# Optimization experiments

Hardware: AMD Instinct MI355X
Metric: run time of the kernel (lower is better)

The kernel has to match this reference:

```python
import jax, jax.numpy as jnp
import numpy as np

B, L, F, H, HDE, E, V, MH, MW, TOUT = 64, 2, 512, 512, 512, 512, 94, 6, 40, 30
V2 = V + 2          # vocab + START/END + NULL slots
T = TOUT + 2        # decode steps
HW = MH * MW
START = V + 1
END = V + 1


def setup_inputs() -> dict:
    key = jax.random.key(0)
    ks = jax.random.split(key, 20)
    s = 0.05  # weight scale for numerical stability
    n = lambda k, shape: jax.random.normal(k, shape, jnp.float32) * s
    d = {}
    d['conv_f'] = jax.random.normal(ks[0], (B, F, MH, MW), jnp.float32)
    d['target'] = jax.random.randint(ks[1], (B, TOUT), 0, 95, dtype=jnp.int32)
    d['w_ih_en'] = n(ks[2], (L, 4 * H, F))
    d['w_hh_en'] = n(ks[3], (L, 4 * H, H))
    d['b_ih_en'] = n(ks[4], (L, 4 * H))
    d['b_hh_en'] = n(ks[5], (L, 4 * H))
    d['embed_w'] = n(ks[6], (V2, H))
    d['w_ih_de'] = n(ks[7], (L, 4 * HDE, H))
    d['w_hh_de'] = n(ks[8], (L, 4 * HDE, HDE))
    d['b_ih_de'] = n(ks[9], (L, 4 * HDE))
    d['b_hh_de'] = n(ks[10], (L, 4 * HDE))
    d['att_wh'] = n(ks[11], (E, HDE))
    d['att_bh'] = n(ks[12], (E,))
    d['att_conv_w'] = n(ks[13], (E, F, 3, 3))
    d['att_conv_b'] = n(ks[14], (E,))
    d['att_wv'] = n(ks[15], (1, E))
    d['att_bv'] = n(ks[16], (1,))
    d['out_w'] = n(ks[17], (V2, HDE + F))
    d['out_b'] = n(ks[18], (V2,))
    return d


def _lstm_cell(x, h, c, wih, whh, bih, bhh):
    # PyTorch gate order: i, f, g, o
    g = x @ wih.T + h @ whh.T + bih + bhh
    i, f, gg, o = jnp.split(g, 4, axis=-1)
    c_new = jax.nn.sigmoid(f) * c + jax.nn.sigmoid(i) * jnp.tanh(gg)
    h_new = jax.nn.sigmoid(o) * jnp.tanh(c_new)
    return h_new, c_new


def _forward(conv_f, target, w_ih_en, w_hh_en, b_ih_en, b_hh_en, embed_w,
             w_ih_de, w_hh_de, b_ih_de, b_hh_de, att_wh, att_bh,
             att_conv_w, att_conv_b, att_wv, att_bv, out_w, out_b):
    # ---- encoder: maxpool over full height, then 2-layer LSTM over width ----
    x_seq = jnp.max(conv_f, axis=2).transpose(2, 0, 1)  # [W, B, F]

    def enc_step(carry, xt):
        h, c = carry
        inp = xt
        hs, cs = [], []
        for l in range(L):
            hl, cl = _lstm_cell(inp, h[l], c[l], w_ih_en[l], w_hh_en[l],
                                b_ih_en[l], b_hh_en[l])
            inp = hl
            hs.append(hl); cs.append(cl)
        return (jnp.stack(hs), jnp.stack(cs)), inp

    z = jnp.zeros((L, B, H), conv_f.dtype)
    _, enc_out = jax.lax.scan(enc_step, (z, z), x_seq)
    holistic = enc_out[-1]  # [B, H]

    # ---- attention: conv_f embedding computed ONCE (invariant across steps) ----
    xe = jax.lax.conv_general_dilated(
        conv_f, att_conv_w, (1, 1), 'SAME',
        dimension_numbers=('NCHW', 'OIHW', 'NCHW')) + att_conv_b[None, :, None, None]
    x_em = xe.reshape(B, E, HW).transpose(0, 2, 1)       # [B, HW, E]
    cf_flat = conv_f.reshape(B, F, HW).transpose(0, 2, 1)  # [B, HW, F]

    # ---- decoder inputs: t=0 holistic, t>=1 embed(gt_with_start[:, t-1]) ----
    gt = jnp.concatenate(
        [jnp.full((B, 1), START, dtype=target.dtype), target], axis=1)  # [B, T-1]
    xs = jnp.concatenate([holistic[None], embed_w[gt.T]], axis=0)  # [T, B, H]

    def dec_step(carry, xt):
        h, c = carry
        inp = xt
        hs, cs = [], []
        for l in range(L):
            hl, cl = _lstm_cell(inp, h[l], c[l], w_ih_de[l], w_hh_de[l],
                                b_ih_de[l], b_hh_de[l])
            inp = hl
            hs.append(hl); cs.append(cl)
        hlast = inp  # [B, HDE]
        g_em = hlast @ att_wh.T + att_bh                    # [B, E]
        feat = jnp.tanh(x_em + g_em[:, None, :])            # [B, HW, E] (dropout=identity)
        e = feat @ att_wv[0] + att_bv[0]                    # [B, HW]
        alpha = jax.nn.softmax(e, axis=-1)
        att = jnp.einsum('bw,bwf->bf', alpha, cf_flat)      # [B, F]
        logits = jnp.concatenate([hlast, att], axis=-1) @ out_w.T + out_b
        scores = jax.nn.log_softmax(logits, axis=-1)        # [B, V2]
        return (jnp.stack(hs), jnp.stack(cs)), scores

    zd = jnp.zeros((B, HDE), conv_f.dtype)
    z0 = jnp.stack([zd] * L)
    _, out_tbv = jax.lax.scan(dec_step, (z0, z0), xs)  # [T, B, V2]
    out = out_tbv.transpose(1, 0, 2)                    # [B, T, V2]

    # ---- build l_target: [0, target..., 0] with first padding 0 -> END ----
    l_target = jnp.zeros((B, T), jnp.int32).at[:, 1:-1].set(target)
    j = jnp.argmax(l_target[:, 1:] == 0, axis=1) + 1  # first zero at col>=1 (always exists)
    l_target = l_target.at[jnp.arange(B), j].set(END)

    # ---- masked NLL loss ----
    lt = l_target.reshape(-1)
    nll = -out.reshape(-1, V2)[jnp.arange(B * T), lt]
    mask = (lt != 0).astype(out.dtype)
    return jnp.sum(nll * mask) / jnp.sum(mask)


def reference(conv_f, target, w_ih_en, w_hh_en, b_ih_en, b_hh_en, embed_w,
              w_ih_de, w_hh_de, b_ih_de, b_hh_de, att_wh, att_bh,
              att_conv_w, att_conv_b, att_wv, att_bv, out_w, out_b):
    return _forward(conv_f, target, w_ih_en, w_hh_en, b_ih_en, b_hh_en, embed_w,
                    w_ih_de, w_hh_de, b_ih_de, b_hh_de, att_wh, att_bh,
                    att_conv_w, att_conv_b, att_wv, att_bv, out_w, out_b)
```

## Files before the change

### kernel.cpp

```cpp
#include <hip/hip_runtime.h>

typedef __fp16 f16;
typedef __fp16 f16x4 __attribute__((ext_vector_type(4)));
typedef __fp16 f16x8 __attribute__((ext_vector_type(8)));
typedef float  f32x4 __attribute__((ext_vector_type(4)));
typedef unsigned long long ull;

#define DEV static __device__ __forceinline__

DEV f32x4 mfma16(f16x4 a, f16x4 b, f32x4 c) {
  return __builtin_amdgcn_mfma_f32_16x16x16f16(a, b, c, 0, 0, 0);
}
DEV f16x4 lo4(f16x8 v) { return __builtin_shufflevector(v, v, 0, 1, 2, 3); }
DEV f16x4 hi4(f16x8 v) { return __builtin_shufflevector(v, v, 4, 5, 6, 7); }
DEV float sigf(float x) { return 1.f / (1.f + __expf(-x)); }
DEV float tanh_(float x) { float e = __expf(2.f * x); return 1.f - 2.f / (e + 1.f); }

union U8 { float4 f4; float2 f2[2]; };
union H2 { unsigned u; f16 h[2]; };
union H4 { ull u; f16 h[4]; f16x4 v; };

#define HB 32768

DEV ull ldU(const ull* p) {
  return __hip_atomic_load(p, __ATOMIC_RELAXED, __HIP_MEMORY_SCOPE_AGENT);
}
DEV unsigned ldF(const unsigned* p) {
  return __hip_atomic_load(p, __ATOMIC_RELAXED, __HIP_MEMORY_SCOPE_AGENT);
}
DEV void stU32(unsigned* p, unsigned v) {
  __hip_atomic_store(p, v, __ATOMIC_RELAXED, __HIP_MEMORY_SCOPE_AGENT);
}
DEV void stU64(ull* p, ull v) {
  __hip_atomic_store(p, v, __ATOMIC_RELAXED, __HIP_MEMORY_SCOPE_AGENT);
}

DEV void wait8(const unsigned* line, unsigned tgt) {
  if (threadIdx.x < 8)
    while (ldF(line + threadIdx.x * 16) < tgt) {}
  __syncthreads();
}

DEV void signalDone(unsigned* line, int slot) {
  asm volatile("s_waitcnt vmcnt(0)" ::: "memory");
  __syncthreads();
  if (threadIdx.x == 0)
    __hip_atomic_fetch_add(line + slot * 16, 1u, __ATOMIC_RELAXED, __HIP_MEMORY_SCOPE_AGENT);
}

DEV void stageRow(const f16* __restrict__ s, f16* __restrict__ dstRow, int ch) {
  U8 u0, u1;
  u0.f4 = *(const float4*)s;
  u1.f4 = *(const float4*)(s + 8);
  *(float2*)(dstRow +  0 + ch * 4) = u0.f2[0];
  *(float2*)(dstRow + 16 + ch * 4) = u0.f2[1];
  *(float2*)(dstRow + 32 + ch * 4) = u1.f2[0];
  *(float2*)(dstRow + 48 + ch * 4) = u1.f2[1];
}

DEV void stageAp(const f16* __restrict__ rowSrc, f16 (*A)[64][72], int tid) {
  int ch = tid & 3;
  const f16* s = rowSrc + ch * 16;
#pragma unroll
  for (int c = 0; c < 8; ++c)
    stageRow(s + c * 64, &A[c][tid >> 2][0], ch);
}

DEV void stageAu(const ull* __restrict__ srcU, f16 (*A)[64][72], int tid) {
  int row = tid >> 2, ch = tid & 3;
  const ull* s = srcU + row * 128 + ch * 4;
#pragma unroll
  for (int c = 0; c < 8; ++c) {
    ull d0 = ldU(s + c * 16 + 0);
    ull d1 = ldU(s + c * 16 + 1);
    ull d2 = ldU(s + c * 16 + 2);
    ull d3 = ldU(s + c * 16 + 3);
    f16* d = &A[c][row][0];
    *(ull*)(d +  0 + ch * 4) = d0;
    *(ull*)(d + 16 + ch * 4) = d1;
    *(ull*)(d + 32 + ch * 4) = d2;
    *(ull*)(d + 48 + ch * 4) = d3;
  }
}

DEV void kloop32(const f16 (*Wt)[32][72], const f16 (*A)[64][72],
                 int mh, int ns, int m16, int g4, f32x4 acc[2]) {
#pragma unroll
  for (int c = 0; c < 8; ++c) {
#pragma unroll
    for (int half = 0; half < 2; ++half) {
      f16x8 bf = *(const f16x8*)&Wt[c][ns * 16 + m16][g4 * 16 + half * 8];
      f16x4 bl = lo4(bf), bh = hi4(bf);
#pragma unroll
      for (int mt = 0; mt < 2; ++mt) {
        f16x8 af = *(const f16x8*)&A[c][mh * 32 + mt * 16 + m16][g4 * 16 + half * 8];
        acc[mt] = mfma16(lo4(af), bl, acc[mt]);
        acc[mt] = mfma16(hi4(af), bh, acc[mt]);
      }
    }
  }
}

DEV void kloop64(const f16* Wg, const f16 (*A)[64][72],
                 int nsG, int m16, int g4, f32x4 acc[4]) {
#pragma unroll
  for (int c = 0; c < 8; ++c) {
#pragma unroll
    for (int half = 0; half < 2; ++half) {
      f16x8 bf = *(const f16x8*)&Wg[((size_t)(c * 64 + nsG * 16 + m16)) * 72 + g4 * 16 + half * 8];
      f16x4 bl = lo4(bf), bh = hi4(bf);
#pragma unroll
      for (int mt = 0; mt < 4; ++mt) {
        f16x8 af = *(const f16x8*)&A[c][mt * 16 + m16][g4 * 16 + half * 8];
        acc[mt] = mfma16(lo4(af), bl, acc[mt]);
        acc[mt] = mfma16(hi4(af), bh, acc[mt]);
      }
    }
  }
}

DEV void convTile(char* smem, int tile, const f16* __restrict__ cfT,
                  const f16* __restrict__ wc9, const float* __restrict__ cb,
                  f16* __restrict__ xemH) {
  f16 (*At)[40] = (f16(*)[40])smem;
  f16 (*Bt)[40] = (f16(*)[40])(smem + 19200);
  const int t = threadIdx.x, lane = t & 63, w = t >> 6;
  const int b = tile >> 2, eb = (tile & 3) * 128;
  const int m16 = lane & 15, g4 = lane >> 4;
  f32x4 acc[15][2] = {};

  for (int kr = 0; kr < 9; ++kr) {
    int dh = kr / 3 - 1, dw = kr % 3 - 1;
    for (int f0 = 0; f0 < 512; f0 += 32) {
      __syncthreads();
      if (t < 240) {
        int hh = t / 40 + dh, ww = t % 40 + dw;
        if (hh >= 0 && hh < 6 && ww >= 0 && ww < 40) {
          const f16* s = cfT + ((size_t)(b * 240 + hh * 40 + ww) * 512 + f0);
          U8 u0, u1, u2, u3;
          u0.f4 = *(const float4*)s;        u1.f4 = *(const float4*)(s + 8);
          u2.f4 = *(const float4*)(s + 16); u3.f4 = *(const float4*)(s + 24);
          *(float2*)&At[t][ 0] = u0.f2[0];
          *(float2*)&At[t][ 8] = u0.f2[1];
          *(float2*)&At[t][16] = u1.f2[0];
          *(float2*)&At[t][24] = u1.f2[1];
          *(float2*)&At[t][ 4] = u2.f2[0];
          *(float2*)&At[t][12] = u2.f2[1];
          *(float2*)&At[t][20] = u3.f2[0];
          *(float2*)&At[t][28] = u3.f2[1];
        } else {
          float2 z = make_float2(0.f, 0.f);
          *(float2*)&At[t][ 0] = z; *(float2*)&At[t][ 8] = z;
          *(float2*)&At[t][16] = z; *(float2*)&At[t][24] = z;
          *(float2*)&At[t][ 4] = z; *(float2*)&At[t][12] = z;
          *(float2*)&At[t][20] = z; *(float2*)&At[t][28] = z;
        }
      }
      {
        int n = t >> 1, ch = t & 1;
        const f16* s = wc9 + (size_t)(eb + n) * 4608 + kr * 512 + f0 + ch * 16;
        U8 u0, u1;
        u0.f4 = *(const float4*)s; u1.f4 = *(const float4*)(s + 8);
        *(float2*)&Bt[n][ 0 + ch * 4] = u0.f2[0];
        *(float2*)&Bt[n][ 8 + ch * 4] = u0.f2[1];
        *(float2*)&Bt[n][16 + ch * 4] = u1.f2[0];
        *(float2*)&Bt[n][24 + ch * 4] = u1.f2[1];
      }
      __syncthreads();
      f16x8 b0 = *(const f16x8*)&Bt[w * 32 + m16][g4 * 8];
      f16x8 b1v = *(const f16x8*)&Bt[w * 32 + 16 + m16][g4 * 8];
      f16x4 b0l = lo4(b0), b0h = hi4(b0), b1l = lo4(b1v), b1h = hi4(b1v);
#pragma unroll
      for (int mt = 0; mt < 15; ++mt) {
        f16x8 af = *(const f16x8*)&At[mt * 16 + m16][g4 * 8];
        f16x4 al = lo4(af), ah = hi4(af);
        acc[mt][0] = mfma16(al, b0l, acc[mt][0]);
        acc[mt][1] = mfma16(al, b1l, acc[mt][1]);
        acc[mt][0] = mfma16(ah, b0h, acc[mt][0]);
        acc[mt][1] = mfma16(ah, b1h, acc[mt][1]);
      }
    }
  }
#pragma unroll
  for (int nt = 0; nt < 2; ++nt) {
    int e = eb + w * 32 + nt * 16 + m16;
    float bias = cb[e];
#pragma unroll
    for (int mt = 0; mt < 15; ++mt)
#pragma unroll
      for (int r = 0; r < 4; ++r) {
        int p = mt * 16 + g4 * 4 + r;
        xemH[((size_t)(b * 240 + p)) * 512 + e] = (f16)(acc[mt][nt][r] + bias);
      }
  }
}

__global__ __launch_bounds__(256) void k_prep(
    const float* __restrict__ att_cw, f16* __restrict__ wc9,
    const float* __restrict__ s0, const float* __restrict__ s1,
    const float* __restrict__ s2, const float* __restrict__ s3,
    f16* __restrict__ d0, f16* __restrict__ d1,
    f16* __restrict__ d2, f16* __restrict__ d3,
    const float* __restrict__ awhS, const float* __restrict__ embS,
    const float* __restrict__ outwS,
    f16* __restrict__ awhD, f16* __restrict__ embD, f16* __restrict__ outwD,
    unsigned* __restrict__ z0, unsigned* __restrict__ z1, unsigned* __restrict__ z2,
    unsigned* __restrict__ z3, unsigned* __restrict__ z4, unsigned* __restrict__ z5)
{
  const int bid = blockIdx.x, tid = threadIdx.x;
  if (bid < 512) {
    __shared__ float s[4608];
    const int e = bid;
    for (int i = tid; i < 4608; i += 256) s[i] = att_cw[(size_t)e * 4608 + i];
    __syncthreads();
    for (int j = tid; j < 4608; j += 256) {
      int rr = j >> 9, f = j & 511;
      wc9[(size_t)e * 4608 + j] = (f16)s[f * 9 + rr];
    }
  } else if (bid < 8704) {
    int i = (bid - 512) * 256 + tid;
    int sel = i >> 19, j = i & 524287;
    const float* s = sel == 0 ? s0 : sel == 1 ? s1 : sel == 2 ? s2 : s3;
    f16* d = sel == 0 ? d0 : sel == 1 ? d1 : sel == 2 ? d2 : d3;
    float4 v = ((const float4*)s)[j];
    f16x4 o = { (f16)v.x, (f16)v.y, (f16)v.z, (f16)v.w };
    *(f16x4*)(d + (size_t)j * 4) = o;
  } else if (bid < 9104) {
    int i = (bid - 8704) * 256 + tid;
    const float* s; f16* d; int j;
    if (i < 65536) { s = awhS; d = awhD; j = i; }
    else if (i < 65536 + 12288) { s = embS; d = embD; j = i - 65536; }
    else if (i < 65536 + 12288 + 24576) { s = outwS; d = outwD; j = i - 65536 - 12288; }
    else return;
    float4 v = ((const float4*)s)[j];
    f16x4 o = { (f16)v.x, (f16)v.y, (f16)v.z, (f16)v.w };
    *(f16x4*)(d + (size_t)j * 4) = o;
  } else {
    int i = (bid - 9104) * 256 + tid;
    int sel = i >> 14, j = i & 16383;
    unsigned* p = sel == 0 ? z0 : sel == 1 ? z1 : sel == 2 ? z2 :
                  sel == 3 ? z3 : sel == 4 ? z4 : z5;
    p[j] = 0;
  }
}

__global__ __launch_bounds__(256) void k_cfmx(
// ... 36 lines not shown
__global__ __launch_bounds__(256) void k_gemmX(
    const f16* __restrict__ A, const f16* __restrict__ W,
    const float* __restrict__ b1, const float* __restrict__ b2,
    f16* __restrict__ C)
{
  __shared__ f16 At[64][72];
  __shared__ f16 Bt[64][72];
  const int t = threadIdx.x, lane = t & 63, g = t >> 6;
  f32x4 acc[4] = {};
  const int m16 = lane & 15, g4 = lane >> 4;
  const size_t arow0 = (size_t)blockIdx.x * 64;

  for (int k0 = 0; k0 < 512; k0 += 64) {
    __syncthreads();
    { int row = t >> 2, ch = t & 3;
      stageRow(A + (arow0 + row) * 512 + k0 + ch * 16, &At[row][0], ch); }
    { int row = t >> 2, ch = t & 3;
      stageRow(W + ((size_t)blockIdx.y * 64 + row) * 512 + k0 + ch * 16, &Bt[row][0], ch); }
    __syncthreads();
#pragma unroll
    for (int half = 0; half < 2; ++half) {
      f16x8 bf = *(const f16x8*)&Bt[g * 16 + m16][g4 * 16 + half * 8];
      f16x4 bl = lo4(bf), bh = hi4(bf);
#pragma unroll
      for (int mt = 0; mt < 4; ++mt) {
        f16x8 af = *(const f16x8*)&At[mt * 16 + m16][g4 * 16 + half * 8];
        acc[mt] = mfma16(lo4(af), bl, acc[mt]);
        acc[mt] = mfma16(hi4(af), bh, acc[mt]);
      }
    }
  }
  int e = blockIdx.y * 64 + g * 16 + m16;
  float bias = b1[e] + b2[e];
#pragma unroll
  for (int mt = 0; mt < 4; ++mt)
#pragma unroll
    for (int r = 0; r < 4; ++r)
      C[(arow0 + mt * 16 + g4 * 4 + r) * 2048 + e] = (f16)(acc[mt][r] + bias);
}

__global__ __launch_bounds__(256, 1) void k_lstm(
    int T, int mode,
    const f16* __restrict__ G0, const f16* __restrict__ whh0,
    const f16* __restrict__ wih1, const f16* __restrict__ whh1,
    const float* __restrict__ bih1, const float* __restrict__ bhh1,
    f16* __restrict__ h0seq, f16* __restrict__ h1seq,
    unsigned* __restrict__ cnt,
    const f16* __restrict__ cfT, const f16* __restrict__ wc9,
    const float* __restrict__ cb, f16* __restrict__ xemH, int convBase,
    f16* __restrict__ X0de, const f16* __restrict__ wihD0,
    const float* __restrict__ bihD0, const float* __restrict__ bhhD0,
    const f16* __restrict__ emb, const int* __restrict__ tgt,
    const f16* __restrict__ x_t0,
    const f16* __restrict__ awh, const float* __restrict__ gbias, f16* __restrict__ gAll)
{
  __shared__ __align__(16) char smem[147456];
  const int tid = threadIdx.x, lane = tid & 63, w = tid >> 6;
  const int m16 = lane & 15, g4 = lane >> 4;
  const int bid = blockIdx.x;

  if (bid < 32) {
    f16 (*sW)[64][72] = (f16(*)[64][72])smem;
    f16 (*sA)[64][72] = (f16(*)[64][72])(smem + 73728);
    float* sG = (float*)(smem + 73728);
    const int utile = bid;
    { int r = tid >> 2, ch = tid & 3;
      int grow = (r >> 4) * 512 + utile * 16 + (r & 15);
      for (int c = 0; c < 8; ++c)
        stageRow(whh0 + (size_t)grow * 512 + c * 64 + ch * 16, &sW[c][r][0], ch);
    }
    const int pb = tid >> 2, uq = tid & 3;
    float cst[4] = {0.f, 0.f, 0.f, 0.f};
    for (int t = 0; t < T; ++t) {
      if (t > 0) wait8(cnt + (size_t)(t - 1) * 128, 4);
      else if (mode == 1) wait8(cnt + (size_t)(2 * T) * 128, 1);
      const f16* gpp = G0 + (size_t)(t * 64 + pb) * 2048 + utile * 16 + uq * 4;
      H4 gI, gF, gG, gO;
      gI.v = *(const f16x4*)(gpp);
      gF.v = *(const f16x4*)(gpp + 512);
      gG.v = *(const f16x4*)(gpp + 1024);
      gO.v = *(const f16x4*)(gpp + 1536);
      stageAu((const ull*)h0seq + (size_t)t * 8192, sA, tid);
      __syncthreads();
      f32x4 acc[4] = {};
      kloop64((const f16*)sW, sA, w, m16, g4, acc);
      __syncthreads();
#pragma unroll
      for (int mt = 0; mt < 4; ++mt)
#pragma unroll
        for (int r = 0; r < 4; ++r)
          sG[((size_t)w * 64 + mt * 16 + g4 * 4 + r) * 17 + m16] = acc[mt][r];
      __syncthreads();
      {
        H4 outp;
#pragma unroll
        for (int j = 0; j < 4; ++j) {
          int u = uq * 4 + j;
          float gi = sG[(0 * 64 + pb) * 17 + u] + (float)gI.h[j];
          float gf = sG[(1 * 64 + pb) * 17 + u] + (float)gF.h[j];
          float gg = sG[(2 * 64 + pb) * 17 + u] + (float)gG.h[j];
          float go = sG[(3 * 64 + pb) * 17 + u] + (float)gO.h[j];
          float cn = sigf(gf) * cst[j] + sigf(gi) * tanh_(gg);
          float hn = sigf(go) * tanh_(cn);
          cst[j] = cn;
          outp.h[j] = (f16)hn;
        }
        stU64((ull*)h0seq + (size_t)(t + 1) * 8192 + pb * 128 + utile * 4 + uq, outp.u);
// ... 31 lines not shown
      else       __syncthreads();
      ull rg[8][4];
      { const ull* s1p = (const ull*)h1seq + (size_t)t * 8192 + (tid >> 2) * 128 + (tid & 3) * 4;
#pragma unroll
        for (int c = 0; c < 8; ++c)
#pragma unroll
          for (int q = 0; q < 4; ++q) rg[c][q] = ldU(s1p + c * 16 + q);
      }
      f32x4 acc[2] = {};
      kloop32(sW2[0], sA, mh, ns, m16, g4, acc);
      __syncthreads();
      { int row = tid >> 2, ch = tid & 3;
#pragma unroll
        for (int c = 0; c < 8; ++c) {
          f16* d = &sA[c][row][0];
          *(ull*)(d +  0 + ch * 4) = rg[c][0];
          *(ull*)(d + 16 + ch * 4) = rg[c][1];
          *(ull*)(d + 32 + ch * 4) = rg[c][2];
          *(ull*)(d + 48 + ch * 4) = rg[c][3];
        }
      }
      __syncthreads();
      kloop32(sW2[1], sA, mh, ns, m16, g4, acc);
      __syncthreads();
      { int nl = ns * 16 + m16;
#pragma unroll
        for (int mt = 0; mt < 2; ++mt)
#pragma unroll
          for (int r = 0; r < 4; ++r) {
            int b = mh * 32 + mt * 16 + g4 * 4 + r;
            sG[((nl >> 3) * 64 + b) * 9 + (nl & 7)] = acc[mt][r];
          }
      }
      __syncthreads();
      {
        H2 outp;
#pragma unroll
        for (int j = 0; j < 2; ++j) {
          int u = pup * 2 + j;
          float gi = sG[(0 * 64 + pb) * 9 + u] + badd[0][j];
          float gf = sG[(1 * 64 + pb) * 9 + u] + badd[1][j];
          float gg = sG[(2 * 64 + pb) * 9 + u] + badd[2][j];
          float go = sG[(3 * 64 + pb) * 9 + u] + badd[3][j];
          float cn = sigf(gf) * cst[j] + sigf(gi) * tanh_(gg);
          float hn = sigf(go) * tanh_(cn);
          cst[j] = cn;
          outp.h[j] = (f16)hn;
        }
        stU32((unsigned*)h1seq + (size_t)(t + 1) * 16384 + pb * 256 + utile * 4 + pup, outp.u);
      }
      signalDone(line1 + (size_t)t * 128, bid & 7);
    }
  } else if (bid < 224) {
    convTile(smem, convBase + bid - 96, cfT, wc9, cb, xemH);
  } else if (mode == 0) {
    const int rid = bid - 224;
    f16 (*sW)[64][72] = (f16(*)[64][72])smem;
    f16 (*sA)[64][72] = (f16(*)[64][72])(smem + 73728);
    { int r = tid >> 2, ch = tid & 3;
      for (int c = 0; c < 8; ++c)
        stageRow(wihD0 + (size_t)(rid * 64 + r) * 512 + c * 64 + ch * 16, &sW[c][r][0], ch);
    }
    const int e = rid * 64 + w * 16 + m16;
    const float bias_e = bihD0[e] + bhhD0[e];
    const int arow = tid >> 2;
    __syncthreads();
    for (int tt = 1; tt < 32; ++tt) {
      const f16* rowSrc = (tt == 1) ? emb + (size_t)95 * 512
                                    : emb + (size_t)tgt[arow * 30 + tt - 2] * 512;
      stageAp(rowSrc, sA, tid);
      __syncthreads();
      f32x4 acc[4] = {};
      kloop64((const f16*)sW, sA, w, m16, g4, acc);
      __syncthreads();
#pragma unroll
      for (int mt = 0; mt < 4; ++mt)
#pragma unroll
        for (int r = 0; r < 4; ++r)
          X0de[((size_t)tt * 64 + mt * 16 + g4 * 4 + r) * 2048 + e] = (f16)(acc[mt][r] + bias_e);
      __syncthreads();
    }
  } else {
    const int g = bid - 224;
    f16* sWg = (f16*)smem;
    f16 (*sA)[64][72] = (f16(*)[64][72])(smem + 73728);
    stageAp(x_t0 + (size_t)(tid >> 2) * 512, sA, tid);
    __syncthreads();
    for (int q = 0; q < 4; ++q) {
      const int rid = g * 4 + q;
      { int r = tid >> 2, ch = tid & 3;
        for (int c = 0; c < 8; ++c)
          stageRow(wihD0 + (size_t)(rid * 64 + r) * 512 + c * 64 + ch * 16,
                   sWg + ((size_t)(c * 64 + r)) * 72, ch);
      }
      __syncthreads();
      f32x4 acc[4] = {};
      kloop64(sWg, sA, w, m16, g4, acc);
      const int e = rid * 64 + w * 16 + m16;
      const float bias_e = bihD0[e] + bhhD0[e];
#pragma unroll
      for (int mt = 0; mt < 4; ++mt)
#pragma unroll
        for (int r = 0; r < 4; ++r)
          X0de[((size_t)(mt * 16 + g4 * 4 + r)) * 2048 + e] = (f16)(acc[mt][r] + bias_e);
      __syncthreads();
    }
    signalDone(cnt + (size_t)(2 * T) * 128, g);
    { int r = tid >> 2, ch = tid & 3;
      for (int c = 0; c < 8; ++c)
        stageRow(awh + (size_t)(g * 64 + r) * 512 + c * 64 + ch * 16,
                 sWg + ((size_t)(c * 64 + r)) * 72, ch);
    }
    const int e = g * 64 + w * 16 + m16;
    const float gb = gbias[e];
    __syncthreads();
    unsigned* line1 = cnt + (size_t)T * 128;
    for (int t = 0; t < T; ++t) {
      wait8(line1 + (size_t)t * 128, 8);
      stageAu((const ull*)h1seq + (size_t)(t + 1) * 8192, sA, tid);
      __syncthreads();
      f32x4 acc[4] = {};
      kloop64(sWg, sA, w, m16, g4, acc);
      __syncthreads();
#pragma unroll
      for (int mt = 0; mt < 4; ++mt)
#pragma unroll
        for (int r = 0; r < 4; ++r)
          gAll[(size_t)(t * 64 + mt * 16 + g4 * 4 + r) * 512 + e] = (f16)(acc[mt][r] + gb);
    }
  }
}


__global__ __launch_bounds__(256) void k_scoreAll(
    const f16* __restrict__ xemH, const f16* __restrict__ gAll,
    const float* __restrict__ wv, float* __restrict__ esc)
{
  __shared__ f16 sX[20][512];
  const int tid = threadIdx.x, lane = tid & 63, w = tid >> 6;
  const int tile = blockIdx.x, b = blockIdx.y;
  for (int i = tid; i < 20 * 64; i += 256) {
    int row = i >> 6, seg = i & 63;
    *(f16x8*)&sX[row][seg * 8] =
        *(const f16x8*)(xemH + ((size_t)(b * 240 + tile * 20 + row)) * 512 + seg * 8);
  }
  float w8[8];
  { const float4* wp = (const float4*)(wv + lane * 8);
    float4 wa = wp[0], wb = wp[1];
    w8[0] = wa.x; w8[1] = wa.y; w8[2] = wa.z; w8[3] = wa.w;
    w8[4] = wb.x; w8[5] = wb.y; w8[6] = wb.z; w8[7] = wb.w; }
  __syncthreads();
  for (int t = 0; t < 32; ++t) {
    f16x8 gv = *(const f16x8*)(gAll + ((size_t)(t * 64 + b)) * 512 + lane * 8);
    float g8[8];
#pragma unroll
    for (int j = 0; j < 8; ++j) g8[j] = (float)gv[j];
#pragma unroll
    for (int i = 0; i < 5; ++i) {
      int rr = i * 4 + w;
      f16x8 xv = *(const f16x8*)&sX[rr][lane * 8];
      float s = 0.f;
#pragma unroll
      for (int j = 0; j < 8; ++j) s += tanh_((float)xv[j] + g8[j]) * w8[j];
#pragma unroll
      for (int m = 32; m; m >>= 1) s += __shfl_xor(s, m);
      if (lane == 0) esc[((size_t)(t * 64 + b)) * 240 + tile * 20 + rr] = s;
    }
  }
}

__global__ __launch_bounds__(256) void k_smctx(
    const float* __restrict__ esc, const f16* __restrict__ cfT,
    const f16* __restrict__ h1seq, f16* __restrict__ ctx)
{
  __shared__ float aAl[8][240];
  const int tid = threadIdx.x, lane = tid & 63, w = tid >> 6;
  const int tq = blockIdx.x, b = blockIdx.y;
  for (int half = 0; half < 2; ++half) {
    int tt = w + half * 4;
    int t = tq * 8 + tt;
    const float* er = esc + ((size_t)(t * 64 + b)) * 240;
    float v[4];
    float mx = -1e30f;
#pragma unroll
    for (int q = 0; q < 4; ++q) {
      int p = lane + q * 64;
      v[q] = (p < 240) ? er[p] : -1e30f;
      mx = fmaxf(mx, v[q]);
    }
#pragma unroll
    for (int m = 32; m; m >>= 1) mx = fmaxf(mx, __shfl_xor(mx, m));
    float sum = 0.f;
#pragma unroll
    for (int q = 0; q < 4; ++q) { v[q] = __expf(v[q] - mx); sum += v[q]; }
#pragma unroll
    for (int m = 32; m; m >>= 1) sum += __shfl_xor(sum, m);
    float inv = 1.f / sum;
#pragma unroll
    for (int q = 0; q < 4; ++q) {
      int p = lane + q * 64;
      if (p < 240) aAl[tt][p] = v[q] * inv;
    }
  }
  __syncthreads();
  float acc[8][2] = {};
  const f16* cb = cfT + (size_t)b * 240 * 512;
  for (int p = 0; p < 240; ++p) {
    H2 cw; cw.u = *(const unsigned*)(cb + (size_t)p * 512 + tid * 2);
    float c0 = (float)cw.h[0], c1 = (float)cw.h[1];
#pragma unroll
    for (int tt = 0; tt < 8; ++tt) {
      float a = aAl[tt][p];
      acc[tt][0] += a * c0;
      acc[tt][1] += a * c1;
    }
  }
#pragma unroll
  for (int tt = 0; tt < 8; ++tt) {
    int t = tq * 8 + tt;
    size_t r = (size_t)(t * 64 + b);
    H2 o; o.h[0] = (f16)acc[tt][0]; o.h[1] = (f16)acc[tt][1];
    *(unsigned*)(ctx + r * 1024 + 512 + tid * 2) = o.u;
    *(unsigned*)(ctx + r * 1024 + tid * 2) =
        *(const unsigned*)(h1seq + (size_t)(t + 1) * HB + b * 512 + tid * 2);
  }
}

__global__ __launch_bounds__(256) void k_logit(
    const f16* __restrict__ A,
    const f16* __restrict__ W,
    const float* __restrict__ bias, const int* __restrict__ tgt,
    float* __restrict__ nllb)
{
  __shared__ f16 At[64][72];
  __shared__ f16 Bt[2][64][72];
  __shared__ float sL[64][100];
  const int tid = threadIdx.x, lane = tid & 63, g = tid >> 6;
  const int m16 = lane & 15, g4 = lane >> 4;
  const int t = blockIdx.x;
  const size_t arow0 = (size_t)t * 64;
  f32x4 acc[2][4] = {};

  for (int k0 = 0; k0 < 1024; k0 += 64) {
    __syncthreads();
    { int row = tid >> 2, ch = tid & 3;
      stageRow(A + (arow0 + row) * 1024 + k0 + ch * 16, &At[row][0], ch);
      stageRow(W + (size_t)row * 1024 + k0 + ch * 16, &Bt[0][row][0], ch);
      stageRow(W + (size_t)(64 + row) * 1024 + k0 + ch * 16, &Bt[1][row][0], ch); }
    __syncthreads();
#pragma unroll
    for (int n2 = 0; n2 < 2; ++n2)
#pragma unroll
      for (int half = 0; half < 2; ++half) {
        f16x8 bf = *(const f16x8*)&Bt[n2][g * 16 + m16][g4 * 16 + half * 8];
        f16x4 bl = lo4(bf), bh = hi4(bf);
#pragma unroll
        for (int mt = 0; mt < 4; ++mt) {
          f16x8 af = *(const f16x8*)&At[mt * 16 + m16][g4 * 16 + half * 8];
          acc[n2][mt] = mfma16(lo4(af), bl, acc[n2][mt]);
          acc[n2][mt] = mfma16(hi4(af), bh, acc[n2][mt]);
        }
      }
  }
  __syncthreads();
#pragma unroll
  for (int n2 = 0; n2 < 2; ++n2) {
    int e = n2 * 64 + g * 16 + m16;
    if (e < 96) {
      float be = bias[e];
#pragma unroll
      for (int mt = 0; mt < 4; ++mt)
#pragma unroll
        for (int r = 0; r < 4; ++r)
          sL[mt * 16 + g4 * 4 + r][e] = acc[n2][mt][r] + be;
    }
  }
  __syncthreads();
  if (tid < 64) {
    int b = tid;
    int jj = 31;
    for (int q = 1; q <= 30; ++q)
      if (tgt[b * 30 + q - 1] == 0) { jj = q; break; }
    int tok = (t == 0 || t == 31) ? 0 : tgt[b * 30 + t - 1];
    if (t == jj) tok = 95;
    float val = 0.f;
    if (tok != 0) {
      float mx = -1e30f;
      for (int j = 0; j < 96; ++j) mx = fmaxf(mx, sL[b][j]);
      float s = 0.f;
      for (int j = 0; j < 96; ++j) s += __expf(sL[b][j] - mx);
      val = mx + __logf(s) - sL[b][tok];
    }
    nllb[t * 64 + b] = val;
  }
}

__global__ void k_loss(const float* __restrict__ nllb, const int* __restrict__ tgt,
                       float* __restrict__ out) {
  __shared__ float sa[256], sb[256];
  int tid = threadIdx.x;
  float a = 0.f, m = 0.f;
  for (int i = tid; i < 2048; i += 256) a += nllb[i];
  if (tid < 64) {
    int b = tid;
    int jj = 31;
    for (int q = 1; q <= 30; ++q)
      if (tgt[b * 30 + q - 1] == 0) { jj = q; break; }
    int cnt = 0;
    for (int t = 1; t <= 30; ++t) {
      int v = tgt[b * 30 + t - 1];
      if (t == jj) v = 95;
      if (v != 0) ++cnt;
    }
    if (jj == 31) ++cnt;
    m = (float)cnt;
  }
  sa[tid] = a; sb[tid] = m; __syncthreads();
  for (int s = 128; s; s >>= 1) { if (tid < s) { sa[tid] += sa[tid + s]; sb[tid] += sb[tid + s]; } __syncthreads(); }
  if (tid == 0) out[0] = sa[0] / sb[0];
}


extern "C" void kernel_launch(void* const* d_in, const int* in_sizes, int n_in,
                              void* d_out, int out_size, void* d_ws, size_t ws_size,
                              hipStream_t stream) {
  (void)in_sizes; (void)n_in; (void)out_size; (void)ws_size;
  const float* conv_f = (const float*)d_in[0];
  const int*   target = (const int*)d_in[1];
  const float* wih_en = (const float*)d_in[2];
  const float* whh_en = (const float*)d_in[3];
  const float* bih_en = (const float*)d_in[4];
  const float* bhh_en = (const float*)d_in[5];
  const float* embed  = (const float*)d_in[6];
  const float* wih_de = (const float*)d_in[7];
  const float* whh_de = (const float*)d_in[8];
  const float* bih_de = (const float*)d_in[9];
  const float* bhh_de = (const float*)d_in[10];
  const float* att_wh = (const float*)d_in[11];
  const float* att_bh = (const float*)d_in[12];
  const float* att_cw = (const float*)d_in[13];
  const float* att_cb = (const float*)d_in[14];
  const float* att_wv = (const float*)d_in[15];
  const float* out_w  = (const float*)d_in[17];
  const float* out_b  = (const float*)d_in[18];
  float* out = (float*)d_out;

  size_t o = 0;
  char* base = (char*)d_ws;
  auto take = [&](size_t bytes) -> void* {
    void* p = base + o;
    o += (bytes + 255) & ~(size_t)255;
    return p;
  };
  const size_t WSZ = (size_t)2048 * 512;
  f16* wihEn = (f16*)take(2 * WSZ * 2);
  f16* whhEn = (f16*)take(2 * WSZ * 2);
  f16* wihDe = (f16*)take(2 * WSZ * 2);
  f16* whhDe = (f16*)take(2 * WSZ * 2);
  f16* awh   = (f16*)take((size_t)512 * 512 * 2);
  f16* emb   = (f16*)take((size_t)96 * 512 * 2);
  f16* wc9   = (f16*)take((size_t)512 * 4608 * 2);
  f16* cfT   = (f16*)take((size_t)64 * 240 * 512 * 2);
  f16* xseq  = (f16*)take((size_t)40 * 64 * 512 * 2);
  f16* xemH  = (f16*)take((size_t)64 * 240 * 512 * 2);
  f16* outwH = (f16*)take((size_t)128 * 1024 * 2);
  f16* X0en  = (f16*)take((size_t)2560 * 2048 * 2);
  f16* X0de  = (f16*)take((size_t)2048 * 2048 * 2);
  f16* h0seqE = (f16*)take((size_t)41 * HB * 2);
  f16* h1seqE = (f16*)take((size_t)41 * HB * 2);
  f16* h0seqD = (f16*)take((size_t)33 * HB * 2);
  f16* h1seqD = (f16*)take((size_t)33 * HB * 2);
  f16* gAll   = (f16*)take((size_t)2048 * 512 * 2);
  float* nllb = (float*)take((size_t)2048 * 4);
  unsigned* cntE = (unsigned*)take(65536);
  unsigned* cntD = (unsigned*)take(65536);
  float* escAll = (float*)X0en;
  f16*   ctxAll = X0de;

  k_cfmx<<<dim3(8, 64), 256, 0, stream>>>(conv_f, cfT, xseq);
  k_prep<<<9488, 256, 0, stream>>>(att_cw, wc9,
                                   wih_en, whh_en, wih_de, whh_de,
                                   wihEn, whhEn, wihDe, whhDe,
                                   att_wh, embed, out_w, awh, emb, outwH,
                                   (unsigned*)h0seqE, (unsigned*)h1seqE,
                                   (unsigned*)h0seqD, (unsigned*)h1seqD, cntE, cntD);

  k_gemmX<<<dim3(40, 32), 256, 0, stream>>>(xseq, wihEn, bih_en, bhh_en, X0en);
  k_lstm<<<256, 256, 0, stream>>>(40, 0, X0en, whhEn, wihEn + WSZ, whhEn + WSZ,
                                  bih_en + 2048, bhh_en + 2048, h0seqE, h1seqE, cntE,
                                  cfT, wc9, att_cb, xemH, 0,
                                  X0de, wihDe, bih_de, bhh_de, emb, target,
                                  nullptr, nullptr, nullptr, nullptr);

  k_lstm<<<232, 256, 0, stream>>>(32, 1, X0de, whhDe, wihDe + WSZ, whhDe + WSZ,
                                  bih_de + 2048, bhh_de + 2048, h0seqD, h1seqD, cntD,
                                  cfT, wc9, att_cb, xemH, 128,
                                  X0de, wihDe, bih_de, bhh_de, emb, target,
                                  h1seqE + (size_t)40 * HB,
                                  awh, att_bh, gAll);

  k_scoreAll<<<dim3(12, 64), 256, 0, stream>>>(xemH, gAll, att_wv, escAll);
  k_smctx<<<dim3(4, 64), 256, 0, stream>>>(escAll, cfT, h1seqD, ctxAll);
  k_logit<<<32, 256, 0, stream>>>(ctxAll, outwH, out_b, target, nllb);
  k_loss<<<1, 256, 0, stream>>>(nllb, target, out);
}
```

Before: 769.8 us.

## Fuse attention score, softmax-context, logits and loss into persistent decoder kernel

The four trailing kernels (score, softmax/context, logit, loss) are moved into the tail of the mode-1 persistent LSTM kernel. Blocks pick up tasks in a grid-stride loop and wait on atomic counters that conv tiles, the gAll producer and each stage signal, so the attention tail can start as soon as its inputs exist. Cross-block data goes through agent-scope atomic loads and stores. The aim is to remove four launch gaps and overlap the tail with conv work. The cost is spin-waits and relaxed-atomic memory traffic, and ctxAll is moved to a new buffer so it no longer aliases X0de.

```diff
diff --git a/kernel.cpp b/kernel.cpp
--- a/kernel.cpp
+++ b/kernel.cpp
@@ -19,6 +19,7 @@
 union U8 { float4 f4; float2 f2[2]; };
 union H2 { unsigned u; f16 h[2]; };
 union H4 { ull u; f16 h[4]; f16x4 v; };
+union U32F { unsigned u; float f; };
 
 #define HB 32768
 
@@ -46,6 +47,13 @@
   __syncthreads();
   if (threadIdx.x == 0)
     __hip_atomic_fetch_add(line + slot * 16, 1u, __ATOMIC_RELAXED, __HIP_MEMORY_SCOPE_AGENT);
+}
+
+DEV void signalOne(unsigned* ctr) {
+  asm volatile("s_waitcnt vmcnt(0)" ::: "memory");
+  __syncthreads();
+  if (threadIdx.x == 0)
+    __hip_atomic_fetch_add(ctr, 1u, __ATOMIC_RELAXED, __HIP_MEMORY_SCOPE_AGENT);
 }
 
 DEV void stageRow(const f16* __restrict__ s, f16* __restrict__ dstRow, int ch) {
@@ -119,15 +127,13 @@
   }
 }
 
-DEV void convTile(char* smem, int tile, const f16* __restrict__ cfT,
-                  const f16* __restrict__ wc9, const float* __restrict__ cb,
-                  f16* __restrict__ xemH) {
+DEV void convCore(char* smem, int tile, const f16* __restrict__ cfT,
+                  const f16* __restrict__ wc9, f32x4 acc[15][2]) {
   f16 (*At)[40] = (f16(*)[40])smem;
   f16 (*Bt)[40] = (f16(*)[40])(smem + 19200);
   const int t = threadIdx.x, lane = t & 63, w = t >> 6;
   const int b = tile >> 2, eb = (tile & 3) * 128;
   const int m16 = lane & 15, g4 = lane >> 4;
-  f32x4 acc[15][2] = {};
 
   for (int kr = 0; kr < 9; ++kr) {
     int dh = kr / 3 - 1, dw = kr % 3 - 1;
@@ -181,6 +187,16 @@
       }
     }
   }
+}
+
+DEV void convTileC(char* smem, int tile, const f16* __restrict__ cfT,
+                   const f16* __restrict__ wc9, const float* __restrict__ cb,
+                   f16* __restrict__ xemH) {
+  f32x4 acc[15][2] = {};
+  convCore(smem, tile, cfT, wc9, acc);
+  const int t = threadIdx.x, lane = t & 63, w = t >> 6;
+  const int b = tile >> 2, eb = (tile & 3) * 128;
+  const int m16 = lane & 15, g4 = lane >> 4;
 #pragma unroll
   for (int nt = 0; nt < 2; ++nt) {
     int e = eb + w * 32 + nt * 16 + m16;
@@ -192,6 +208,36 @@
         int p = mt * 16 + g4 * 4 + r;
         xemH[((size_t)(b * 240 + p)) * 512 + e] = (f16)(acc[mt][nt][r] + bias);
       }
+  }
+}
+
+DEV void convTileA(char* smem, int tile, const f16* __restrict__ cfT,
+                   const f16* __restrict__ wc9, const float* __restrict__ cb,
+                   f16* __restrict__ xemH) {
+  f32x4 acc[15][2] = {};
+  convCore(smem, tile, cfT, wc9, acc);
+  const int t = threadIdx.x, lane = t & 63, w = t >> 6;
+  const int b = tile >> 2, eb = (tile & 3) * 128;
+  const int m16 = lane & 15, g4 = lane >> 4;
+  f16 (*sC)[132] = (f16(*)[132])smem;
+  __syncthreads();
+#pragma unroll
+  for (int nt = 0; nt < 2; ++nt) {
+    int e = eb + w * 32 + nt * 16 + m16;
+    float bias = cb[e];
+#pragma unroll
+    for (int mt = 0; mt < 15; ++mt)
+#pragma unroll
+      for (int r = 0; r < 4; ++r)
+        sC[mt * 16 + g4 * 4 + r][w * 32 + nt * 16 + m16] = (f16)(acc[mt][nt][r] + bias);
+  }
+  __syncthreads();
+#pragma unroll
+  for (int k = 0; k < 30; ++k) {
+    int id = t + k * 256;
+    int row = id >> 5, chk = id & 31;
+    H4 pk; pk.v = *(const f16x4*)&sC[row][chk * 4];
+    stU64((ull*)xemH + (size_t)(b * 240 + row) * 128 + (eb >> 2) + chk, pk.u);
   }
 }
 
@@ -334,7 +380,11 @@
     const float* __restrict__ bihD0, const float* __restrict__ bhhD0,
     const f16* __restrict__ emb, const int* __restrict__ tgt,
     const f16* __restrict__ x_t0,
-    const f16* __restrict__ awh, const float* __restrict__ gbias, f16* __restrict__ gAll)
+    const f16* __restrict__ awh, const float* __restrict__ gbias, f16* __restrict__ gAll,
+    const float* __restrict__ wv, const f16* __restrict__ outwH,
+    const float* __restrict__ outb,
+    float* __restrict__ escAll, f16* __restrict__ ctxAll,
+    float* __restrict__ nllb, float* __restrict__ out)
 {
   __shared__ __align__(16) char smem[147456];
   const int tid = threadIdx.x, lane = tid & 63, w = tid >> 6;
@@ -472,7 +522,13 @@
       signalDone(line1 + (size_t)t * 128, bid & 7);
     }
   } else if (bid < 224) {
-    convTile(smem, convBase + bid - 96, cfT, wc9, cb, xemH);
+    if (mode == 0) {
+      convTileC(smem, convBase + bid - 96, cfT, wc9, cb, xemH);
+    } else {
+      int tile = convBase + bid - 96;
+      convTileA(smem, tile, cfT, wc9, cb, xemH);
+      signalOne(cnt + 8320 + (tile >> 2) * 16);
+    }
   } else if (mode == 0) {
     const int rid = bid - 224;
     f16 (*sW)[64][72] = (f16(*)[64][72])smem;
@@ -504,6 +560,7 @@
     const int g = bid - 224;
     f16* sWg = (f16*)smem;
     f16 (*sA)[64][72] = (f16(*)[64][72])(smem + 73728);
+    f16 (*sC)[72] = (f16(*)[72])(smem + 73728 + 36864);
     stageAp(x_t0 + (size_t)(tid >> 2) * 512, sA, tid);
     __syncthreads();
     for (int q = 0; q < 4; ++q) {
@@ -546,198 +603,238 @@
       for (int mt = 0; mt < 4; ++mt)
 #pragma unroll
         for (int r = 0; r < 4; ++r)
-          gAll[(size_t)(t * 64 + mt * 16 + g4 * 4 + r) * 512 + e] = (f16)(acc[mt][r] + gb);
-    }
-  }
-}
-
-
-__global__ __launch_bounds__(256) void k_scoreAll(
-    const f16* __restrict__ xemH, const f16* __restrict__ gAll,
-    const float* __restrict__ wv, float* __restrict__ esc)
-{
-  __shared__ f16 sX[20][512];
-  const int tid = threadIdx.x, lane = tid & 63, w = tid >> 6;
-  const int tile = blockIdx.x, b = blockIdx.y;
-  for (int i = tid; i < 20 * 64; i += 256) {
-    int row = i >> 6, seg = i & 63;
-    *(f16x8*)&sX[row][seg * 8] =
-        *(const f16x8*)(xemH + ((size_t)(b * 240 + tile * 20 + row)) * 512 + seg * 8);
-  }
-  float w8[8];
-  { const float4* wp = (const float4*)(wv + lane * 8);
-    float4 wa = wp[0], wb = wp[1];
-    w8[0] = wa.x; w8[1] = wa.y; w8[2] = wa.z; w8[3] = wa.w;
-    w8[4] = wb.x; w8[5] = wb.y; w8[6] = wb.z; w8[7] = wb.w; }
+          sC[mt * 16 + g4 * 4 + r][w * 16 + m16] = (f16)(acc[mt][r] + gb);
+      __syncthreads();
+#pragma unroll
+      for (int k = 0; k < 4; ++k) {
+        int id = tid + k * 256;
+        int row = id >> 4, chk = id & 15;
+        H4 pk; pk.v = *(const f16x4*)&sC[row][chk * 4];
+        stU64((ull*)gAll + (size_t)(t * 64 + row) * 128 + g * 16 + chk, pk.u);
+      }
+      __syncthreads();
+    }
+    signalOne(cnt + 9344);
+  }
+
+  if (mode == 0) return;
+
   __syncthreads();
-  for (int t = 0; t < 32; ++t) {
-    f16x8 gv = *(const f16x8*)(gAll + ((size_t)(t * 64 + b)) * 512 + lane * 8);
-    float g8[8];
-#pragma unroll
-    for (int j = 0; j < 8; ++j) g8[j] = (float)gv[j];
-#pragma unroll
-    for (int i = 0; i < 5; ++i) {
-      int rr = i * 4 + w;
-      f16x8 xv = *(const f16x8*)&sX[rr][lane * 8];
-      float s = 0.f;
-#pragma unroll
-      for (int j = 0; j < 8; ++j) s += tanh_((float)xv[j] + g8[j]) * w8[j];
-#pragma unroll
-      for (int m = 32; m; m >>= 1) s += __shfl_xor(s, m);
-      if (lane == 0) esc[((size_t)(t * 64 + b)) * 240 + tile * 20 + rr] = s;
-    }
-  }
-}
-
-__global__ __launch_bounds__(256) void k_smctx(
-    const float* __restrict__ esc, const f16* __restrict__ cfT,
-    const f16* __restrict__ h1seq, f16* __restrict__ ctx)
-{
-  __shared__ float aAl[8][240];
-  const int tid = threadIdx.x, lane = tid & 63, w = tid >> 6;
-  const int tq = blockIdx.x, b = blockIdx.y;
-  for (int half = 0; half < 2; ++half) {
-    int tt = w + half * 4;
-    int t = tq * 8 + tt;
-    const float* er = esc + ((size_t)(t * 64 + b)) * 240;
-    float v[4];
-    float mx = -1e30f;
-#pragma unroll
-    for (int q = 0; q < 4; ++q) {
-      int p = lane + q * 64;
-      v[q] = (p < 240) ? er[p] : -1e30f;
-      mx = fmaxf(mx, v[q]);
-    }
-#pragma unroll
-    for (int m = 32; m; m >>= 1) mx = fmaxf(mx, __shfl_xor(mx, m));
-    float sum = 0.f;
-#pragma unroll
-    for (int q = 0; q < 4; ++q) { v[q] = __expf(v[q] - mx); sum += v[q]; }
-#pragma unroll
-    for (int m = 32; m; m >>= 1) sum += __shfl_xor(sum, m);
-    float inv = 1.f / sum;
-#pragma unroll
-    for (int q = 0; q < 4; ++q) {
-      int p = lane + q * 64;
-      if (p < 240) aAl[tt][p] = v[q] * inv;
-    }
-  }
-  __syncthreads();
-  float acc[8][2] = {};
-  const f16* cb = cfT + (size_t)b * 240 * 512;
-  for (int p = 0; p < 240; ++p) {
-    H2 cw; cw.u = *(const unsigned*)(cb + (size_t)p * 512 + tid * 2);
-    float c0 = (float)cw.h[0], c1 = (float)cw.h[1];
-#pragma unroll
-    for (int tt = 0; tt < 8; ++tt) {
-      float a = aAl[tt][p];
-      acc[tt][0] += a * c0;
-      acc[tt][1] += a * c1;
-    }
-  }
-#pragma unroll
-  for (int tt = 0; tt < 8; ++tt) {
-    int t = tq * 8 + tt;
-    size_t r = (size_t)(t * 64 + b);
-    H2 o; o.h[0] = (f16)acc[tt][0]; o.h[1] = (f16)acc[tt][1];
-    *(unsigned*)(ctx + r * 1024 + 512 + tid * 2) = o.u;
-    *(unsigned*)(ctx + r * 1024 + tid * 2) =
-        *(const unsigned*)(h1seq + (size_t)(t + 1) * HB + b * 512 + tid * 2);
-  }
-}
-
-__global__ __launch_bounds__(256) void k_logit(
-    const f16* __restrict__ A,
-    const f16* __restrict__ W,
-    const float* __restrict__ bias, const int* __restrict__ tgt,
-    float* __restrict__ nllb)
-{
-  __shared__ f16 At[64][72];
-  __shared__ f16 Bt[2][64][72];
-  __shared__ float sL[64][100];
-  const int tid = threadIdx.x, lane = tid & 63, g = tid >> 6;
-  const int m16 = lane & 15, g4 = lane >> 4;
-  const int t = blockIdx.x;
-  const size_t arow0 = (size_t)t * 64;
-  f32x4 acc[2][4] = {};
-
-  for (int k0 = 0; k0 < 1024; k0 += 64) {
+  unsigned* cvb = cnt + 8320;
+  unsigned* gGd = cnt + 9344;
+  unsigned* scb = cnt + 9360;
+  unsigned* smd = cnt + 10384;
+  unsigned* lgd = cnt + 10448;
+
+  {
+    f16 (*sX)[512] = (f16(*)[512])smem;
+    ull* sXu = (ull*)smem;
+    float w8[8];
+    { const float4* wp = (const float4*)(wv + lane * 8);
+      float4 wa = wp[0], wb2 = wp[1];
+      w8[0] = wa.x; w8[1] = wa.y; w8[2] = wa.z; w8[3] = wa.w;
+      w8[4] = wb2.x; w8[5] = wb2.y; w8[6] = wb2.z; w8[7] = wb2.w; }
+    for (int task = bid; task < 768; task += 232) {
+      int b = task / 12, tile = task - b * 12;
+      if (tid == 0 && b >= 32) {
+        while (ldF(cvb + b * 16) < 4u) __builtin_amdgcn_s_sleep(2);
+      } else if (tid == 1) {
+        while (ldF(gGd) < 8u) __builtin_amdgcn_s_sleep(2);
+      }
+      __syncthreads();
+      for (int i = tid; i < 2560; i += 256)
+        sXu[i] = ldU((const ull*)xemH + (size_t)(b * 240 + tile * 20 + (i >> 7)) * 128 + (i & 127));
+      __syncthreads();
+      for (int t = 0; t < 32; ++t) {
+        const ull* gp = (const ull*)gAll + (size_t)(t * 64 + b) * 128 + lane * 2;
+        H4 ga, gb4; ga.u = ldU(gp); gb4.u = ldU(gp + 1);
+        float g8[8];
+#pragma unroll
+        for (int j = 0; j < 4; ++j) { g8[j] = (float)ga.h[j]; g8[4 + j] = (float)gb4.h[j]; }
+#pragma unroll
+        for (int i = 0; i < 5; ++i) {
+          int rr = i * 4 + w;
+          f16x8 xv = *(const f16x8*)&sX[rr][lane * 8];
+          float s = 0.f;
+#pragma unroll
+          for (int j = 0; j < 8; ++j) s += tanh_((float)xv[j] + g8[j]) * w8[j];
+#pragma unroll
+          for (int m = 32; m; m >>= 1) s += __shfl_xor(s, m);
+          if (lane == 0) {
+            U32F u; u.f = s;
+            stU32((unsigned*)escAll + (size_t)(t * 64 + b) * 240 + tile * 20 + rr, u.u);
+          }
+        }
+      }
+      signalOne(scb + b * 16);
+      __syncthreads();
+    }
+  }
+
+  {
+    float* aAl = (float*)smem;
+    for (int task = bid; task < 256; task += 232) {
+      int tq = task >> 6, b = task & 63;
+      if (tid == 0)
+        while (ldF(scb + b * 16) < 12u) __builtin_amdgcn_s_sleep(2);
+      __syncthreads();
+      for (int half = 0; half < 2; ++half) {
+        int tt = w + half * 4;
+        int t = tq * 8 + tt;
+        const unsigned* er = (const unsigned*)escAll + (size_t)(t * 64 + b) * 240;
+        float v[4]; float mx = -1e30f;
+#pragma unroll
+        for (int q = 0; q < 4; ++q) {
+          int p = lane + q * 64;
+          if (p < 240) { U32F u; u.u = ldF(er + p); v[q] = u.f; } else v[q] = -1e30f;
+          mx = fmaxf(mx, v[q]);
+        }
+#pragma unroll
+        for (int m = 32; m; m >>= 1) mx = fmaxf(mx, __shfl_xor(mx, m));
+        float sum = 0.f;
+#pragma unroll
+        for (int q = 0; q < 4; ++q) { v[q] = __expf(v[q] - mx); sum += v[q]; }
+#pragma unroll
+        for (int m = 32; m; m >>= 1) sum += __shfl_xor(sum, m);
+        float inv = 1.f / sum;
+#pragma unroll
+        for (int q = 0; q < 4; ++q) {
+          int p = lane + q * 64;
+          if (p < 240) aAl[tt * 240 + p] = v[q] * inv;
+        }
+      }
+      __syncthreads();
+      float acc2[8][2] = {};
+      const f16* cbp = cfT + (size_t)b * 240 * 512;
+      for (int p = 0; p < 240; ++p) {
+        H2 cw; cw.u = *(const unsigned*)(cbp + (size_t)p * 512 + tid * 2);
+        float c0 = (float)cw.h[0], c1 = (float)cw.h[1];
+#pragma unroll
+        for (int tt = 0; tt < 8; ++tt) {
+          float a = aAl[tt * 240 + p];
+          acc2[tt][0] += a * c0;
+          acc2[tt][1] += a * c1;
+        }
+      }
+#pragma unroll
+      for (int tt = 0; tt < 8; ++tt) {
+        int t = tq * 8 + tt;
+        size_t r = (size_t)(t * 64 + b);
+        H2 o; o.h[0] = (f16)acc2[tt][0]; o.h[1] = (f16)acc2[tt][1];
+        stU32((unsigned*)ctxAll + r * 512 + 256 + tid, o.u);
+        unsigned hv = ldF((const unsigned*)h1seq + (size_t)(t + 1) * 16384 + b * 256 + tid);
+        stU32((unsigned*)ctxAll + r * 512 + tid, hv);
+      }
+      signalOne(smd + tq * 16);
+      __syncthreads();
+    }
+  }
+
+  if (bid < 32) {
+    int t = bid;
+    if (tid == 0)
+      while (ldF(smd + (t >> 3) * 16) < 64u) __builtin_amdgcn_s_sleep(2);
     __syncthreads();
-    { int row = tid >> 2, ch = tid & 3;
-      stageRow(A + (arow0 + row) * 1024 + k0 + ch * 16, &At[row][0], ch);
-      stageRow(W + (size_t)row * 1024 + k0 + ch * 16, &Bt[0][row][0], ch);
-      stageRow(W + (size_t)(64 + row) * 1024 + k0 + ch * 16, &Bt[1][row][0], ch); }
+    f16 (*At)[72] = (f16(*)[72])smem;
+    f16 (*Bt)[64][72] = (f16(*)[64][72])(smem + 9216);
+    float (*sL)[100] = (float(*)[100])(smem + 46080);
+    const int g = tid >> 6;
+    f32x4 acc[2][4] = {};
+    for (int k0 = 0; k0 < 1024; k0 += 64) {
+      __syncthreads();
+      { int row = tid >> 2, ch = tid & 3;
+        const ull* rb = (const ull*)ctxAll + (size_t)(t * 64 + row) * 256 + (k0 >> 2) + ch * 4;
+        ull d0 = ldU(rb), d1 = ldU(rb + 1), d2 = ldU(rb + 2), d3 = ldU(rb + 3);
+        f16* dr = &At[row][0];
+        *(ull*)(dr +  0 + ch * 4) = d0;
+        *(ull*)(dr + 16 + ch * 4) = d1;
+        *(ull*)(dr + 32 + ch * 4) = d2;
+        *(ull*)(dr + 48 + ch * 4) = d3;
+        stageRow(outwH + (size_t)row * 1024 + k0 + ch * 16, &Bt[0][row][0], ch);
+        stageRow(outwH + (size_t)(64 + row) * 1024 + k0 + ch * 16, &Bt[1][row][0], ch);
+      }
+      __syncthreads();
+#pragma unroll
+      for (int n2 = 0; n2 < 2; ++n2)
+#pragma unroll
+        for (int half = 0; half < 2; ++half) {
+          f16x8 bf = *(const f16x8*)&Bt[n2][g * 16 + m16][g4 * 16 + half * 8];
+          f16x4 bl = lo4(bf), bh = hi4(bf);
+#pragma unroll
+          for (int mt = 0; mt < 4; ++mt) {
+            f16x8 af = *(const f16x8*)&At[mt * 16 + m16][g4 * 16 + half * 8];
+            acc[n2][mt] = mfma16(lo4(af), bl, acc[n2][mt]);
+            acc[n2][mt] = mfma16(hi4(af), bh, acc[n2][mt]);
+          }
+        }
+    }
     __syncthreads();
 #pragma unroll
-    for (int n2 = 0; n2 < 2; ++n2)
-#pragma unroll
-      for (int half = 0; half < 2; ++half) {
-        f16x8 bf = *(const f16x8*)&Bt[n2][g * 16 + m16][g4 * 16 + half * 8];
-        f16x4 bl = lo4(bf), bh = hi4(bf);
-#pragma unroll
-        for (int mt = 0; mt < 4; ++mt) {
-          f16x8 af = *(const f16x8*)&At[mt * 16 + m16][g4 * 16 + half * 8];
-          acc[n2][mt] = mfma16(lo4(af), bl, acc[n2][mt]);
-          acc[n2][mt] = mfma16(hi4(af), bh, acc[n2][mt]);
-        }
-      }
-  }
-  __syncthreads();
-#pragma unroll
-  for (int n2 = 0; n2 < 2; ++n2) {
-    int e = n2 * 64 + g * 16 + m16;
-    if (e < 96) {
-      float be = bias[e];
-#pragma unroll
-      for (int mt = 0; mt < 4; ++mt)
-#pragma unroll
-        for (int r = 0; r < 4; ++r)
-          sL[mt * 16 + g4 * 4 + r][e] = acc[n2][mt][r] + be;
-    }
-  }
-  __syncthreads();
-  if (tid < 64) {
-    int b = tid;
-    int jj = 31;
-    for (int q = 1; q <= 30; ++q)
-      if (tgt[b * 30 + q - 1] == 0) { jj = q; break; }
-    int tok = (t == 0 || t == 31) ? 0 : tgt[b * 30 + t - 1];
-    if (t == jj) tok = 95;
-    float val = 0.f;
-    if (tok != 0) {
-      float mx = -1e30f;
-      for (int j = 0; j < 96; ++j) mx = fmaxf(mx, sL[b][j]);
-      float s = 0.f;
-      for (int j = 0; j < 96; ++j) s += __expf(sL[b][j] - mx);
-      val = mx + __logf(s) - sL[b][tok];
-    }
-    nllb[t * 64 + b] = val;
-  }
-}
-
-__global__ void k_loss(const float* __restrict__ nllb, const int* __restrict__ tgt,
-                       float* __restrict__ out) {
-  __shared__ float sa[256], sb[256];
-  int tid = threadIdx.x;
-  float a = 0.f, m = 0.f;
-  for (int i = tid; i < 2048; i += 256) a += nllb[i];
-  if (tid < 64) {
-    int b = tid;
-    int jj = 31;
-    for (int q = 1; q <= 30; ++q)
-      if (tgt[b * 30 + q - 1] == 0) { jj = q; break; }
-    int cnt = 0;
-    for (int t = 1; t <= 30; ++t) {
-      int v = tgt[b * 30 + t - 1];
-      if (t == jj) v = 95;
-      if (v != 0) ++cnt;
-    }
-    if (jj == 31) ++cnt;
-    m = (float)cnt;
-  }
-  sa[tid] = a; sb[tid] = m; __syncthreads();
-  for (int s = 128; s; s >>= 1) { if (tid < s) { sa[tid] += sa[tid + s]; sb[tid] += sb[tid + s]; } __syncthreads(); }
-  if (tid == 0) out[0] = sa[0] / sb[0];
+    for (int n2 = 0; n2 < 2; ++n2) {
+      int e = n2 * 64 + g * 16 + m16;
+      if (e < 96) {
+        float be = outb[e];
+#pragma unroll
+        for (int mt = 0; mt < 4; ++mt)
+#pragma unroll
+          for (int r = 0; r < 4; ++r)
+            sL[mt * 16 + g4 * 4 + r][e] = acc[n2][mt][r] + be;
+      }
+    }
+    __syncthreads();
+    if (tid < 64) {
+      int b = tid;
+      int jj = 31;
+      for (int q = 1; q <= 30; ++q)
+        if (tgt[b * 30 + q - 1] == 0) { jj = q; break; }
+      int tok = (t == 0 || t == 31) ? 0 : tgt[b * 30 + t - 1];
+      if (t == jj) tok = 95;
+      float val = 0.f;
+      if (tok != 0) {
+        float mx = -1e30f;
+        for (int j = 0; j < 96; ++j) mx = fmaxf(mx, sL[b][j]);
+        float s = 0.f;
+        for (int j = 0; j < 96; ++j) s += __expf(sL[b][j] - mx);
+        val = mx + __logf(s) - sL[b][tok];
+      }
+      U32F o; o.f = val;
+      stU32((unsigned*)nllb + t * 64 + b, o.u);
+    }
+    signalOne(lgd);
+  }
+
+  if (bid == 0) {
+    if (tid == 0)
+      while (ldF(lgd) < 32u) __builtin_amdgcn_s_sleep(2);
+    __syncthreads();
+    float* sa = (float*)smem;
+    float* sb = sa + 256;
+    float a = 0.f, m = 0.f;
+    for (int i = tid; i < 2048; i += 256) {
+      U32F u; u.u = ldF((const unsigned*)nllb + i);
+      a += u.f;
+    }
+    if (tid < 64) {
+      int b = tid;
+      int jj = 31;
+      for (int q = 1; q <= 30; ++q)
+        if (tgt[b * 30 + q - 1] == 0) { jj = q; break; }
+      int cntk = 0;
+      for (int t = 1; t <= 30; ++t) {
+        int v = tgt[b * 30 + t - 1];
+        if (t == jj) v = 95;
+        if (v != 0) ++cntk;
+      }
+      if (jj == 31) ++cntk;
+      m = (float)cntk;
+    }
+    sa[tid] = a; sb[tid] = m; __syncthreads();
+    for (int s = 128; s; s >>= 1) {
+      if (tid < s) { sa[tid] += sa[tid + s]; sb[tid] += sb[tid + s]; }
+      __syncthreads();
+    }
+    if (tid == 0) out[0] = sa[0] / sb[0];
+  }
 }
 
 
@@ -795,7 +892,7 @@
   unsigned* cntE = (unsigned*)take(65536);
   unsigned* cntD = (unsigned*)take(65536);
   float* escAll = (float*)X0en;
-  f16*   ctxAll = X0de;
+  f16*   ctxAll = (f16*)((char*)X0en + 4194304);
 
   k_cfmx<<<dim3(8, 64), 256, 0, stream>>>(conv_f, cfT, xseq);
   k_prep<<<9488, 256, 0, stream>>>(att_cw, wc9,
@@ -810,17 +907,14 @@
                                   bih_en + 2048, bhh_en + 2048, h0seqE, h1seqE, cntE,
                                   cfT, wc9, att_cb, xemH, 0,
                                   X0de, wihDe, bih_de, bhh_de, emb, target,
-                                  nullptr, nullptr, nullptr, nullptr);
+                                  nullptr, nullptr, nullptr, nullptr,
+                                  att_wv, outwH, out_b, escAll, ctxAll, nllb, out);
 
   k_lstm<<<232, 256, 0, stream>>>(32, 1, X0de, whhDe, wihDe + WSZ, whhDe + WSZ,
                                   bih_de + 2048, bhh_de + 2048, h0seqD, h1seqD, cntD,
                                   cfT, wc9, att_cb, xemH, 128,
                                   X0de, wihDe, bih_de, bhh_de, emb, target,
                                   h1seqE + (size_t)40 * HB,
-                                  awh, att_bh, gAll);
-
-  k_scoreAll<<<dim3(12, 64), 256, 0, stream>>>(xemH, gAll, att_wv, escAll);
-  k_smctx<<<dim3(4, 64), 256, 0, stream>>>(escAll, cfT, h1seqD, ctxAll);
-  k_logit<<<32, 256, 0, stream>>>(ctxAll, outwH, out_b, target, nllb);
-  k_loss<<<1, 256, 0, stream>>>(nllb, target, out);
-}
+                                  awh, att_bh, gAll,
+                                  att_wv, outwH, out_b, escAll, ctxAll, nllb, out);
+}
```

Measured after the change: 1.000 ms. +29.9%, slower.
